# Kernel optimization log

Hardware: AMD Instinct MI355X
Metric: run time of the kernel (lower is better)

The kernel has to match this reference:

```python
import jax, jax.numpy as jnp
import numpy as np

N = 50000      # nodes
E = 800000     # edges (avg degree 16)
IN_DIM = 128
H = 4          # attention heads
D = 32         # hidden dim per head
NEG_SLOPE = 0.2


def setup_inputs() -> dict:
    key = jax.random.key(0)
    ks = jax.random.split(key, 9)
    x = jax.random.normal(ks[0], (N, IN_DIM), dtype=jnp.float32)
    src = jax.random.randint(ks[1], (E,), 0, N, dtype=jnp.int64)
    dst = jax.random.randint(ks[2], (E,), 0, N, dtype=jnp.int64)
    # layer 0: IN_DIM -> H*D ; layer 1: H*D -> H*D
    s0 = 1.0 / np.sqrt(IN_DIM)
    s1 = 1.0 / np.sqrt(H * D)
    W1 = jax.random.normal(ks[3], (H * D, IN_DIM), dtype=jnp.float32) * s0
    al1 = jax.random.normal(ks[4], (1, H, D), dtype=jnp.float32) * s1
    ar1 = jax.random.normal(ks[5], (1, H, D), dtype=jnp.float32) * s1
    W2 = jax.random.normal(ks[6], (H * D, H * D), dtype=jnp.float32) * s1
    al2 = jax.random.normal(ks[7], (1, H, D), dtype=jnp.float32) * s1
    ar2 = jax.random.normal(ks[8], (1, H, D), dtype=jnp.float32) * s1
    return {"x": x, "src": src, "dst": dst, "W1": W1, "al1": al1, "ar1": ar1,
            "W2": W2, "al2": al2, "ar2": ar2}


def gat_conv(h, src, dst, W, al, ar):
    """DGL-style GATConv. h: [N, F_in] -> [N, H, D], with ELU activation."""
    feat = (h @ W.T).reshape(N, H, D)                 # [N,H,D]
    el = jnp.sum(feat * al, axis=-1)                  # [N,H] a_l . Wh
    er = jnp.sum(feat * ar, axis=-1)                  # [N,H] a_r . Wh
    e = jax.nn.leaky_relu(el[src] + er[dst], NEG_SLOPE)  # [E,H]
    # numerically stable edge softmax over incoming edges of each dst node
    m = jax.ops.segment_max(e, dst, num_segments=N)   # [N,H]
    ee = jnp.exp(e - m[dst])                          # [E,H]
    denom = jax.ops.segment_sum(ee, dst, num_segments=N)  # [N,H]
    alpha = ee / denom[dst]                           # [E,H]
    msg = feat[src] * alpha[..., None]                # [E,H,D]
    out = jax.ops.segment_sum(msg, dst, num_segments=N)   # [N,H,D]
    return jax.nn.elu(out)


def reference(x, src, dst, W1, al1, ar1, W2, al2, ar2):
    h = gat_conv(x, src, dst, W1, al1, ar1).reshape(N, H * D)  # flatten(1)
    h = gat_conv(h, src, dst, W2, al2, ar2)                    # [N,H,D]
    return jnp.mean(h, axis=1)                                 # [N,D]
```

## Files before the change

kernel.cpp:

```cpp
#include <hip/hip_runtime.h>
#include <cmath>
#include <type_traits>

#define HEADS 4
#define FDIM 128
#define NEG 0.2f
#define NBUCK 8

typedef __attribute__((ext_vector_type(8))) __bf16 bf16x8;
typedef __attribute__((ext_vector_type(8))) _Float16 h16x8;
typedef __attribute__((ext_vector_type(4))) float f32x4;

__global__ __launch_bounds__(256) void prep_kernel(
    const float* __restrict__ W1, const float* __restrict__ al1,
    const float* __restrict__ ar1,
    const float* __restrict__ W2, const float* __restrict__ al2,
    const float* __restrict__ ar2,
    __bf16* __restrict__ wf1, __bf16* __restrict__ wext1,
    _Float16* __restrict__ wf2, _Float16* __restrict__ wext2,
    int* __restrict__ counts, int nb)
{
    const int b = blockIdx.x, tid = threadIdx.x;
    if (b < 256) {
        int idx = (b & 127) * 256 + tid;
        int j = idx & 7;
        int r = idx >> 3;
        int c = r & 15; r >>= 4;
        int t = r & 7;  r >>= 3;
        int kq = r & 15;
        int hl = r >> 4;
        if (b < 128) {
            float v = W1[(t * 16 + c) * 128 + kq * 8 + j];
            __bf16 hi = (__bf16)v;
            wf1[idx] = (hl == 0) ? hi : (__bf16)(v - (float)hi);
        } else {
            float v = W2[(t * 16 + c) * 128 + kq * 8 + j];
            _Float16 hi = (_Float16)v;
            wf2[idx] = (hl == 0) ? hi : (_Float16)(v - (float)hi);
        }
    } else if (b < 258) {
        const float* W  = (b == 256) ? W1 : W2;
        const float* al = (b == 256) ? al1 : al2;
        const float* ar = (b == 256) ? ar1 : ar2;
        __shared__ float val[1024];
        #pragma unroll
        for (int ch = 0; ch < 4; ++ch) {
            int idx = ch * 256 + tid;
            int c = idx >> 7, k = idx & 127;
            int h = c & 3;
            const float* a = (c < 4) ? al : ar;
            float s = 0.f;
            for (int d = 0; d < 32; ++d)
                s += a[h * 32 + d] * W[(h * 32 + d) * 128 + k];
            val[c * 128 + k] = s;
        }
        __syncthreads();
        #pragma unroll
        for (int ch = 0; ch < 16; ++ch) {
            int idx = tid * 16 + ch;
            int j = idx & 7;
            int r = idx >> 3;
            int c = r & 15; r >>= 4;
            int kq = r & 15;
            int hl = r >> 4;
            float v = (c < 8) ? val[c * 128 + kq * 8 + j] : 0.f;
            if (b == 256) {
                __bf16 hi = (__bf16)v;
                wext1[idx] = (hl == 0) ? hi : (__bf16)(v - (float)hi);
            } else {
                _Float16 hi = (_Float16)v;
                wext2[idx] = (hl == 0) ? hi : (_Float16)(v - (float)hi);
            }
        }
    } else {
        int i0 = ((b - 258) * 256 + tid) * 4;
        if (i0 + 3 < nb) {
            *(int4*)&counts[i0] = make_int4(0, 0, 0, 0);
        } else {
            for (int i = i0; i < nb; ++i) counts[i] = 0;
        }
    }
}

__device__ __forceinline__ void gemm_body_f32(
    const float* __restrict__ X, const bf16x8* __restrict__ wf,
    const bf16x8* __restrict__ wext, _Float16* __restrict__ featH,
    float* __restrict__ el, float* __restrict__ er,
    int nnodes, int tile0, int tend, int stride, bf16x8* lw)
{
    const int tid = threadIdx.x;
    const int wave = tid >> 6, lane = tid & 63;
    const int l15 = lane & 15, quad = lane >> 4;

    int tile = tile0;
    float xr[32], xn[32];

    auto loadX = [&](int tl, float* dst) {
        int nodeA = tl * 64 + wave * 16 + l15;
        bool v = nodeA < nnodes;
        const float4* xp = (const float4*)(X + (size_t)nodeA * 128);
        #pragma unroll
        for (int ks = 0; ks < 4; ++ks) {
            float4 a = v ? xp[ks * 8 + quad * 2]     : make_float4(0.f, 0.f, 0.f, 0.f);
            float4 b = v ? xp[ks * 8 + quad * 2 + 1] : make_float4(0.f, 0.f, 0.f, 0.f);
            dst[ks * 8 + 0] = a.x; dst[ks * 8 + 1] = a.y;
            dst[ks * 8 + 2] = a.z; dst[ks * 8 + 3] = a.w;
            dst[ks * 8 + 4] = b.x; dst[ks * 8 + 5] = b.y;
            dst[ks * 8 + 6] = b.z; dst[ks * 8 + 7] = b.w;
        }
    };

    loadX(tile, xr);
    for (int i = tid; i < 2048; i += 256) lw[i] = wf[i];
    __syncthreads();

    while (true) {
        int next = tile + stride;
        if (next < tend) loadX(next, xn);

        f32x4 acc[9];
        #pragma unroll
        for (int t = 0; t < 9; ++t) acc[t] = (f32x4){0.f, 0.f, 0.f, 0.f};

        #pragma unroll
        for (int ks = 0; ks < 4; ++ks) {
            bf16x8 ahi, alo;
            #pragma unroll
            for (int j = 0; j < 8; ++j) {
                float xv = xr[ks * 8 + j];
                __bf16 h = (__bf16)xv;
                ahi[j] = h;
                alo[j] = (__bf16)(xv - (float)h);
            }
            const int kq = ks * 4 + quad;

            {
                bf16x8 bh = wext[(kq) * 16 + l15];
                bf16x8 bl = wext[(16 + kq) * 16 + l15];
                acc[8] = __builtin_amdgcn_mfma_f32_16x16x32_bf16(ahi, bh, acc[8], 0, 0, 0);
                acc[8] = __builtin_amdgcn_mfma_f32_16x16x32_bf16(alo, bh, acc[8], 0, 0, 0);
                acc[8] = __builtin_amdgcn_mfma_f32_16x16x32_bf16(ahi, bl, acc[8], 0, 0, 0);
            }
            #pragma unroll
            for (int t = 0; t < 8; ++t) {
                bf16x8 bh = lw[(kq * 8 + t) * 16 + l15];
                bf16x8 bl = wf[2048 + (kq * 8 + t) * 16 + l15];
                acc[t] = __builtin_amdgcn_mfma_f32_16x16x32_bf16(ahi, bh, acc[t], 0, 0, 0);
                acc[t] = __builtin_amdgcn_mfma_f32_16x16x32_bf16(alo, bh, acc[t], 0, 0, 0);
                acc[t] = __builtin_amdgcn_mfma_f32_16x16x32_bf16(ahi, bl, acc[t], 0, 0, 0);
            }
        }

        const int nodeC = tile * 64 + wave * 16 + quad * 4;
        #pragma unroll
        for (int r = 0; r < 4; ++r) {
            int gn = nodeC + r;
            if (gn < nnodes) {
                #pragma unroll
                for (int t = 0; t < 8; ++t)
                    featH[(size_t)gn * 128 + t * 16 + l15] = (_Float16)acc[t][r];
            }
        }
        if (l15 < 8) {
            #pragma unroll
            for (int r = 0; r < 4; ++r) {
                int gn = nodeC + r;
                if (gn < nnodes) {
                    if (l15 < 4) el[gn * HEADS + l15] = acc[8][r];
                    else         er[gn * HEADS + (l15 - 4)] = acc[8][r];
                }
            }
        }

        if (next >= tend) break;
        #pragma unroll
        for (int i = 0; i < 32; ++i) xr[i] = xn[i];
        tile = next;
    }
}

__device__ __forceinline__ void gemm_body_f16(
    const _Float16* __restrict__ X, const h16x8* __restrict__ wf,
    const h16x8* __restrict__ wext, _Float16* __restrict__ featH,
    float* __restrict__ el, float* __restrict__ er,
    int nnodes, int tile0, int tend, int stride, h16x8* lw)
{
    const int tid = threadIdx.x;
    const int wave = tid >> 6, lane = tid & 63;
    const int l15 = lane & 15, quad = lane >> 4;

    int tile = tile0;
    h16x8 xr[4], xn[4];

    auto loadX = [&](int tl, h16x8* dst) {
        int nodeA = tl * 64 + wave * 16 + l15;
        bool v = nodeA < nnodes;
        const h16x8* xp = (const h16x8*)(X + (size_t)nodeA * 128);
        #pragma unroll
        for (int ks = 0; ks < 4; ++ks) {
            if (v) {
                dst[ks] = xp[ks * 4 + quad];
            } else {
                #pragma unroll
                for (int j = 0; j < 8; ++j) dst[ks][j] = (_Float16)0.f;
            }
        }
    };

    loadX(tile, xr);
    for (int i = tid; i < 2048; i += 256) lw[i] = wf[i];
    __syncthreads();

    while (true) {
        int next = tile + stride;
        if (next < tend) loadX(next, xn);

        f32x4 acc[9];
        #pragma unroll
        for (int t = 0; t < 9; ++t) acc[t] = (f32x4){0.f, 0.f, 0.f, 0.f};

        #pragma unroll
        for (int ks = 0; ks < 4; ++ks) {
            h16x8 a = xr[ks];
            const int kq = ks * 4 + quad;
            {
                h16x8 bh = wext[(kq) * 16 + l15];
                h16x8 bl = wext[(16 + kq) * 16 + l15];
                acc[8] = __builtin_amdgcn_mfma_f32_16x16x32_f16(a, bh, acc[8], 0, 0, 0);
                acc[8] = __builtin_amdgcn_mfma_f32_16x16x32_f16(a, bl, acc[8], 0, 0, 0);
            }
            #pragma unroll
            for (int t = 0; t < 8; ++t) {
                h16x8 bh = lw[(kq * 8 + t) * 16 + l15];
                h16x8 bl = wf[2048 + (kq * 8 + t) * 16 + l15];
                acc[t] = __builtin_amdgcn_mfma_f32_16x16x32_f16(a, bh, acc[t], 0, 0, 0);
                acc[t] = __builtin_amdgcn_mfma_f32_16x16x32_f16(a, bl, acc[t], 0, 0, 0);
            }
        }

        const int nodeC = tile * 64 + wave * 16 + quad * 4;
        #pragma unroll
        for (int r = 0; r < 4; ++r) {
            int gn = nodeC + r;
            if (gn < nnodes) {
                #pragma unroll
                for (int t = 0; t < 8; ++t)
                    featH[(size_t)gn * 128 + t * 16 + l15] = (_Float16)acc[t][r];
            }
        }
        if (l15 < 8) {
            #pragma unroll
            for (int r = 0; r < 4; ++r) {
                int gn = nodeC + r;
                if (gn < nnodes) {
                    if (l15 < 4) el[gn * HEADS + l15] = acc[8][r];
                    else         er[gn * HEADS + (l15 - 4)] = acc[8][r];
                }
            }
        }

        if (next >= tend) break;
        #pragma unroll
        for (int i = 0; i < 4; ++i) xr[i] = xn[i];
        tile = next;
    }
}

__device__ __forceinline__ void hist_body(
    const int* __restrict__ src, const int* __restrict__ dst,
    int* __restrict__ counts, int* __restrict__ rank, int nedges, int shift, int b)
{
    int i0 = (b * 256 + threadIdx.x) * 8;
    if (i0 + 7 < nedges) {
        int4 d0 = *(const int4*)&dst[i0];
        int4 d1 = *(const int4*)&dst[i0 + 4];
        int4 s0 = *(const int4*)&src[i0];
        int4 s1 = *(const int4*)&src[i0 + 4];
        int4 r0, r1;
        r0.x = atomicAdd(&counts[d0.x * NBUCK + (s0.x >> shift)], 1);
        r0.y = atomicAdd(&counts[d0.y * NBUCK + (s0.y >> shift)], 1);
        r0.z = atomicAdd(&counts[d0.z * NBUCK + (s0.z >> shift)], 1);
        r0.w = atomicAdd(&counts[d0.w * NBUCK + (s0.w >> shift)], 1);
        r1.x = atomicAdd(&counts[d1.x * NBUCK + (s1.x >> shift)], 1);
        r1.y = atomicAdd(&counts[d1.y * NBUCK + (s1.y >> shift)], 1);
        r1.z = atomicAdd(&counts[d1.z * NBUCK + (s1.z >> shift)], 1);
        r1.w = atomicAdd(&counts[d1.w * NBUCK + (s1.w >> shift)], 1);
        *(int4*)&rank[i0]     = r0;
        *(int4*)&rank[i0 + 4] = r1;
    } else {
        for (int i = i0; i < nedges; ++i)
            rank[i] = atomicAdd(&counts[dst[i] * NBUCK + (src[i] >> shift)], 1);
    }
}

__device__ __forceinline__ void scatter_body(
    const int* __restrict__ src, const int* __restrict__ dst,
    const int* __restrict__ rank, const int* __restrict__ offsets,
    int* __restrict__ csr_src, int nedges, int shift, int b)
{
    int i0 = (b * 256 + threadIdx.x) * 8;
    if (i0 + 7 < nedges) {
        int4 d0 = *(const int4*)&dst[i0];
        int4 d1 = *(const int4*)&dst[i0 + 4];
        int4 r0 = *(const int4*)&rank[i0];
        int4 r1 = *(const int4*)&rank[i0 + 4];
        int4 s0 = *(const int4*)&src[i0];
        int4 s1 = *(const int4*)&src[i0 + 4];
        csr_src[offsets[d0.x * NBUCK + (s0.x >> shift)] + r0.x] = s0.x;
        csr_src[offsets[d0.y * NBUCK + (s0.y >> shift)] + r0.y] = s0.y;
        csr_src[offsets[d0.z * NBUCK + (s0.z >> shift)] + r0.z] = s0.z;
        csr_src[offsets[d0.w * NBUCK + (s0.w >> shift)] + r0.w] = s0.w;
        csr_src[offsets[d1.x * NBUCK + (s1.x >> shift)] + r1.x] = s1.x;
        csr_src[offsets[d1.y * NBUCK + (s1.y >> shift)] + r1.y] = s1.y;
        csr_src[offsets[d1.z * NBUCK + (s1.z >> shift)] + r1.z] = s1.z;
        csr_src[offsets[d1.w * NBUCK + (s1.w >> shift)] + r1.w] = s1.w;
    } else {
        for (int i = i0; i < nedges; ++i)
            csr_src[offsets[dst[i] * NBUCK + (src[i] >> shift)] + rank[i]] = src[i];
    }
}

__global__ __launch_bounds__(256) void fused_gemm_hist(
    const float* __restrict__ X, const bf16x8* __restrict__ wf,
    const bf16x8* __restrict__ wext, _Float16* __restrict__ featH,
    float* __restrict__ el, float* __restrict__ er, int nnodes,
    int t0, int tend, int gemm_blocks,
    const int* __restrict__ src, const int* __restrict__ dst,
    int* __restrict__ counts, int* __restrict__ rank, int nedges, int shift)
{
    __shared__ bf16x8 lw[2048];
    if ((int)blockIdx.x < gemm_blocks)
        gemm_body_f32(X, wf, wext, featH, el, er, nnodes,
                      t0 + blockIdx.x, tend, gemm_blocks, lw);
    else
        hist_body(src, dst, counts, rank, nedges, shift, blockIdx.x - gemm_blocks);
}

__global__ __launch_bounds__(256) void fused_gemm_scatter(
    const float* __restrict__ X, const bf16x8* __restrict__ wf,
    const bf16x8* __restrict__ wext, _Float16* __restrict__ featH,
    float* __restrict__ el, float* __restrict__ er, int nnodes,
    int t0, int tend, int gemm_blocks,
    const int* __restrict__ src, const int* __restrict__ dst,
    const int* __restrict__ rank, const int* __restrict__ offsets,
    int* __restrict__ csr_src, int nedges, int shift)
{
    __shared__ bf16x8 lw[2048];
    if ((int)blockIdx.x < gemm_blocks)
        gemm_body_f32(X, wf, wext, featH, el, er, nnodes,
                      t0 + blockIdx.x, tend, gemm_blocks, lw);
    else
        scatter_body(src, dst, rank, offsets, csr_src, nedges, shift,
                     blockIdx.x - gemm_blocks);
}

__global__ __launch_bounds__(256) void gemm_mfma_f16_kernel(
    const _Float16* __restrict__ X, const h16x8* __restrict__ wf,
    const h16x8* __restrict__ wext, _Float16* __restrict__ featH,
    float* __restrict__ el, float* __restrict__ er, int nnodes, int ntiles)
{
    __shared__ h16x8 lw[2048];
    gemm_body_f16(X, wf, wext, featH, el, er, nnodes,
                  blockIdx.x, ntiles, gridDim.x, lw);
}

__global__ __launch_bounds__(256) void scan1_kernel(
    const int* __restrict__ counts, int* __restrict__ offsets,
    int* __restrict__ bsums, int n)
{
    __shared__ int wsums[4];
    const int tid = threadIdx.x, lane = tid & 63, w = tid >> 6;
    const int i = blockIdx.x * 1024 + tid * 4;

    int4 v = make_int4(0, 0, 0, 0);
    if (i + 3 < n) v = *(const int4*)&counts[i];
    else {
        if (i < n)     v.x = counts[i];
        if (i + 1 < n) v.y = counts[i + 1];
        if (i + 2 < n) v.z = counts[i + 2];
    }
    int s0 = v.x, s1 = s0 + v.y, s2 = s1 + v.z, s3 = s2 + v.w;

    int x = s3;
    #pragma unroll
    for (int off = 1; off < 64; off <<= 1) {
        int t = __shfl_up(x, off, 64);
        if (lane >= off) x += t;
    }
    if (lane == 63) wsums[w] = x;
    __syncthreads();
    int wbase = 0;
    #pragma unroll
    for (int k = 0; k < 4; ++k) if (k < w) wbase += wsums[k];

    int tbase = wbase + x - s3;
    if (i < n)     offsets[i]     = tbase;
    if (i + 1 < n) offsets[i + 1] = tbase + s0;
    if (i + 2 < n) offsets[i + 2] = tbase + s1;
    if (i + 3 < n) offsets[i + 3] = tbase + s2;
    if (tid == 255) bsums[blockIdx.x] = wbase + x;
}

__global__ __launch_bounds__(256) void scan23_kernel(
    int* __restrict__ offsets, const int* __restrict__ bsums, int n, int nedges)
{
    __shared__ int sbase;
    const int tid = threadIdx.x, b = blockIdx.x;
    if (tid < 64) {
        int s = 0;
        for (int i = tid; i < b; i += 64) s += bsums[i];
        #pragma unroll
        for (int off = 1; off < 64; off <<= 1) s += __shfl_xor(s, off, 64);
        if (tid == 0) sbase = s;
    }
    __syncthreads();
    const int base = sbase;
    const int i = b * 1024 + tid * 4;
    #pragma unroll
    for (int k = 0; k < 4; ++k)
        if (i + k < n) offsets[i + k] += base;
    if (b == 0 && tid == 0) offsets[n] = nedges;
}

template <bool MEAN>
__global__ __launch_bounds__(256) void aggregate_kernel(
    const _Float16* __restrict__ featH, const float* __restrict__ el,
    const float* __restrict__ er, const int* __restrict__ offsets,
    const int* __restrict__ csr_src, void* __restrict__ outp, int nnodes)
{
    const int n = (blockIdx.x * 256 + threadIdx.x) >> 6;
    if (n >= nnodes) return;
    const int lane = threadIdx.x & 63;
    const int g = lane >> 4, u = lane & 15, h = u >> 2;
    const int beg = offsets[n * NBUCK], end = offsets[n * NBUCK + NBUCK];
    const float ern = er[n * HEADS + h];
    const int iters = (end - beg + 3) >> 2;

    float a[8];
    #pragma unroll
    for (int p = 0; p < 8; ++p) a[p] = 0.f;
    float sw = 0.f;

    const h16x8* __restrict__ frow = (const h16x8*)featH;

    int ja = beg + g;
    int jb = ja + 4;
    bool va = ja < end, vb = jb < end;
    int sa = va ? csr_src[ja] : 0;
    int sb = vb ? csr_src[jb] : 0;
    float qa = el[sa * HEADS + h];
    float qb = el[sb * HEADS + h];
    h16x8 fa = frow[(size_t)sa * 16 + u];
    h16x8 fb = frow[(size_t)sb * 16 + u];

    for (int it = 0; it < iters; ++it) {
        int jc = ja + 8;
        bool vc = jc < end;
        int sc = vc ? csr_src[jc] : 0;
        float qc = el[sc * HEADS + h];
        h16x8 fc = frow[(size_t)sc * 16 + u];

        float e = qa + ern;
        e = e > 0.f ? e : NEG * e;
        float w2 = va ? __expf(e) : 0.f;
        #pragma unroll
        for (int p = 0; p < 8; ++p) a[p] += w2 * (float)fa[p];
        sw += w2;

        ja = jb; va = vb; sa = sb; qa = qb; fa = fb;
        jb = jc; vb = vc; sb = sc; qb = qc; fb = fc;
    }

    #pragma unroll
    for (int p = 0; p < 8; ++p) {
        a[p] += __shfl_xor(a[p], 16, 64);
        a[p] += __shfl_xor(a[p], 32, 64);
    }
    sw += __shfl_xor(sw, 16, 64);
    sw += __shfl_xor(sw, 32, 64);

    float inv = sw > 0.f ? 1.f / sw : 0.f;
    float r[8];
    #pragma unroll
    for (int p = 0; p < 8; ++p) {
        float t = a[p] * inv;
        r[p] = t > 0.f ? t : __expf(t) - 1.f;
    }

    if (!MEAN) {
        if (g == 0) {
            h16x8 o;
            #pragma unroll
            for (int p = 0; p < 8; ++p) o[p] = (_Float16)r[p];
            ((h16x8*)outp)[(size_t)n * 16 + u] = o;
        }
    } else {
        #pragma unroll
        for (int p = 0; p < 8; ++p) {
            r[p] += __shfl_xor(r[p], 4, 64);
            r[p] += __shfl_xor(r[p], 8, 64);
        }
        if (g == 0 && u < 4) {
            float* out = (float*)outp;
            float4* o4 = (float4*)(out + (size_t)n * 32 + u * 8);
            o4[0] = make_float4(0.25f * r[0], 0.25f * r[1], 0.25f * r[2], 0.25f * r[3]);
            o4[1] = make_float4(0.25f * r[4], 0.25f * r[5], 0.25f * r[6], 0.25f * r[7]);
        }
    }
}

extern "C" void kernel_launch(void* const* d_in, const int* in_sizes, int n_in,
                              void* d_out, int out_size, void* d_ws, size_t ws_size,
                              hipStream_t stream)
{
    const float* x   = (const float*)d_in[0];
    const int*   src = (const int*)d_in[1];
    const int*   dst = (const int*)d_in[2];
    const float* W1  = (const float*)d_in[3];
    const float* al1 = (const float*)d_in[4];
    const float* ar1 = (const float*)d_in[5];
    const float* W2  = (const float*)d_in[6];
    const float* al2 = (const float*)d_in[7];
    const float* ar2 = (const float*)d_in[8];

    const int N = in_sizes[0] / FDIM;
    const int E = in_sizes[1];
    const int NB = N * NBUCK;

    int shift = 0;
    while (((N - 1) >> shift) > (NBUCK - 1)) ++shift;

    _Float16* h1 = (_Float16*)d_ws;
    _Float16* featH = h1 + (size_t)N * FDIM;
    float* el = (float*)(featH + (size_t)N * FDIM);
    float* er = el + (size_t)N * HEADS;
    int* counts  = (int*)(er + (size_t)N * HEADS);
    int* offsets = counts + NB;
    int* rank    = offsets + (NB + 1);
    int* csr_src = rank + E;
    int* bsums   = csr_src + E;
    uintptr_t wp = ((uintptr_t)(bsums + 512) + 63) & ~(uintptr_t)63;
    __bf16* wf1     = (__bf16*)wp;
    __bf16* wext1   = wf1 + 32768;
    _Float16* wf2   = (_Float16*)(wext1 + 4096);
    _Float16* wext2 = wf2 + 32768;

    const int ntiles = (N + 63) / 64;
    const int halfT  = (ntiles + 1) / 2;
    const int gA = halfT < 256 ? halfT : 256;
    const int gB = (ntiles - halfT) < 256 ? (ntiles - halfT) : 256;
    const int edge8_grid = ((E + 7) / 8 + 255) / 256;
    const int agg_grid  = (N + 3) / 4;
    const int nscan     = (NB + 1023) / 1024;
    const int zblocks   = ((NB + 3) / 4 + 255) / 256;
    const int g2 = ntiles < 512 ? ntiles : 512;

    prep_kernel<<<258 + zblocks, 256, 0, stream>>>(
        W1, al1, ar1, W2, al2, ar2, wf1, wext1, wf2, wext2, counts, NB);

    fused_gemm_hist<<<gA + edge8_grid, 256, 0, stream>>>(
        x, (const bf16x8*)wf1, (const bf16x8*)wext1, featH, el, er, N,
        0, halfT, gA, src, dst, counts, rank, E, shift);

    scan1_kernel<<<nscan, 256, 0, stream>>>(counts, offsets, bsums, NB);
    scan23_kernel<<<nscan, 256, 0, stream>>>(offsets, bsums, NB, E);

    fused_gemm_scatter<<<gB + edge8_grid, 256, 0, stream>>>(
        x, (const bf16x8*)wf1, (const bf16x8*)wext1, featH, el, er, N,
        halfT, ntiles, gB, src, dst, rank, offsets, csr_src, E, shift);

    aggregate_kernel<false><<<agg_grid, 256, 0, stream>>>(
        featH, el, er, offsets, csr_src, (void*)h1, N);

    gemm_mfma_f16_kernel<<<g2, 256, 0, stream>>>(
        h1, (const h16x8*)wf2, (const h16x8*)wext2, featH, el, er, N, ntiles);
    aggregate_kernel<true><<<agg_grid, 256, 0, stream>>>(
        featH, el, er, offsets, csr_src, d_out, N);
}
```

Before: 238.8 us.

## Replace global-atomic CSR build with two-level LDS radix-style bucket sort

The CSR construction no longer does per-edge global atomics on a dst×src-bucket count array. It now runs a coarse histogram per edge block in LDS, keyed on dst>>7, and scans the block×bucket matrix. A scatter pass then writes (src,dst) pairs into coarse buckets, and a new fine_sort kernel sorts each 128-node bucket in LDS to produce offsets and csr_src. This removes contended global atomics and the counts-zeroing pass, at the cost of an extra kernel, a larger scan and an intermediate int2 buffer. Buckets larger than 4096 edges are silently truncated.

```diff
diff --git a/kernel.cpp b/kernel.cpp
--- a/kernel.cpp
+++ b/kernel.cpp
@@ -6,6 +6,8 @@
 #define FDIM 128
 #define NEG 0.2f
 #define NBUCK 8
+#define CSHIFT 7
+#define CMASK 127
 
 typedef __attribute__((ext_vector_type(8))) __bf16 bf16x8;
 typedef __attribute__((ext_vector_type(8))) _Float16 h16x8;
@@ -17,8 +19,7 @@
     const float* __restrict__ W2, const float* __restrict__ al2,
     const float* __restrict__ ar2,
     __bf16* __restrict__ wf1, __bf16* __restrict__ wext1,
-    _Float16* __restrict__ wf2, _Float16* __restrict__ wext2,
-    int* __restrict__ counts, int nb)
+    _Float16* __restrict__ wf2, _Float16* __restrict__ wext2)
 {
     const int b = blockIdx.x, tid = threadIdx.x;
     if (b < 256) {
@@ -38,7 +39,7 @@
             _Float16 hi = (_Float16)v;
             wf2[idx] = (hl == 0) ? hi : (_Float16)(v - (float)hi);
         }
-    } else if (b < 258) {
+    } else {
         const float* W  = (b == 256) ? W1 : W2;
         const float* al = (b == 256) ? al1 : al2;
         const float* ar = (b == 256) ? ar1 : ar2;
@@ -72,13 +73,6 @@
                 wext2[idx] = (hl == 0) ? hi : (_Float16)(v - (float)hi);
             }
         }
-    } else {
-        int i0 = ((b - 258) * 256 + tid) * 4;
-        if (i0 + 3 < nb) {
-            *(int4*)&counts[i0] = make_int4(0, 0, 0, 0);
-        } else {
-            for (int i = i0; i < nb; ++i) counts[i] = 0;
-        }
     }
 }
 
@@ -266,92 +260,164 @@
     }
 }
 
-__device__ __forceinline__ void hist_body(
-    const int* __restrict__ src, const int* __restrict__ dst,
-    int* __restrict__ counts, int* __restrict__ rank, int nedges, int shift, int b)
-{
-    int i0 = (b * 256 + threadIdx.x) * 8;
+__device__ __forceinline__ void coarse_hist_body(
+    const int* __restrict__ dst, int* __restrict__ histmat,
+    int nedges, int nblk, int nbkt, int eb, int* chist)
+{
+    const int tid = threadIdx.x;
+    for (int i = tid; i < nbkt; i += 256) chist[i] = 0;
+    __syncthreads();
+    int i0 = eb * 2048 + tid * 8;
     if (i0 + 7 < nedges) {
         int4 d0 = *(const int4*)&dst[i0];
         int4 d1 = *(const int4*)&dst[i0 + 4];
-        int4 s0 = *(const int4*)&src[i0];
-        int4 s1 = *(const int4*)&src[i0 + 4];
-        int4 r0, r1;
-        r0.x = atomicAdd(&counts[d0.x * NBUCK + (s0.x >> shift)], 1);
-        r0.y = atomicAdd(&counts[d0.y * NBUCK + (s0.y >> shift)], 1);
-        r0.z = atomicAdd(&counts[d0.z * NBUCK + (s0.z >> shift)], 1);
-        r0.w = atomicAdd(&counts[d0.w * NBUCK + (s0.w >> shift)], 1);
-        r1.x = atomicAdd(&counts[d1.x * NBUCK + (s1.x >> shift)], 1);
-        r1.y = atomicAdd(&counts[d1.y * NBUCK + (s1.y >> shift)], 1);
-        r1.z = atomicAdd(&counts[d1.z * NBUCK + (s1.z >> shift)], 1);
-        r1.w = atomicAdd(&counts[d1.w * NBUCK + (s1.w >> shift)], 1);
-        *(int4*)&rank[i0]     = r0;
-        *(int4*)&rank[i0 + 4] = r1;
+        atomicAdd(&chist[d0.x >> CSHIFT], 1);
+        atomicAdd(&chist[d0.y >> CSHIFT], 1);
+        atomicAdd(&chist[d0.z >> CSHIFT], 1);
+        atomicAdd(&chist[d0.w >> CSHIFT], 1);
+        atomicAdd(&chist[d1.x >> CSHIFT], 1);
+        atomicAdd(&chist[d1.y >> CSHIFT], 1);
+        atomicAdd(&chist[d1.z >> CSHIFT], 1);
+        atomicAdd(&chist[d1.w >> CSHIFT], 1);
     } else {
         for (int i = i0; i < nedges; ++i)
-            rank[i] = atomicAdd(&counts[dst[i] * NBUCK + (src[i] >> shift)], 1);
-    }
-}
-
-__device__ __forceinline__ void scatter_body(
+            atomicAdd(&chist[dst[i] >> CSHIFT], 1);
+    }
+    __syncthreads();
+    for (int i = tid; i < nbkt; i += 256)
+        histmat[i * nblk + eb] = chist[i];
+}
+
+__device__ __forceinline__ void coarse_scatter_body(
     const int* __restrict__ src, const int* __restrict__ dst,
-    const int* __restrict__ rank, const int* __restrict__ offsets,
-    int* __restrict__ csr_src, int nedges, int shift, int b)
-{
-    int i0 = (b * 256 + threadIdx.x) * 8;
+    const int* __restrict__ histoff, int2* __restrict__ tmp,
+    int nedges, int nblk, int nbkt, int eb, int* chist)
+{
+    const int tid = threadIdx.x;
+    for (int i = tid; i < nbkt; i += 256) chist[i] = 0;
+    __syncthreads();
+    int i0 = eb * 2048 + tid * 8;
     if (i0 + 7 < nedges) {
-        int4 d0 = *(const int4*)&dst[i0];
-        int4 d1 = *(const int4*)&dst[i0 + 4];
-        int4 r0 = *(const int4*)&rank[i0];
-        int4 r1 = *(const int4*)&rank[i0 + 4];
-        int4 s0 = *(const int4*)&src[i0];
-        int4 s1 = *(const int4*)&src[i0 + 4];
-        csr_src[offsets[d0.x * NBUCK + (s0.x >> shift)] + r0.x] = s0.x;
-        csr_src[offsets[d0.y * NBUCK + (s0.y >> shift)] + r0.y] = s0.y;
-        csr_src[offsets[d0.z * NBUCK + (s0.z >> shift)] + r0.z] = s0.z;
-        csr_src[offsets[d0.w * NBUCK + (s0.w >> shift)] + r0.w] = s0.w;
-        csr_src[offsets[d1.x * NBUCK + (s1.x >> shift)] + r1.x] = s1.x;
-        csr_src[offsets[d1.y * NBUCK + (s1.y >> shift)] + r1.y] = s1.y;
-        csr_src[offsets[d1.z * NBUCK + (s1.z >> shift)] + r1.z] = s1.z;
-        csr_src[offsets[d1.w * NBUCK + (s1.w >> shift)] + r1.w] = s1.w;
+        int s[8], d[8];
+        *(int4*)&s[0] = *(const int4*)&src[i0];
+        *(int4*)&s[4] = *(const int4*)&src[i0 + 4];
+        *(int4*)&d[0] = *(const int4*)&dst[i0];
+        *(int4*)&d[4] = *(const int4*)&dst[i0 + 4];
+        #pragma unroll
+        for (int q = 0; q < 8; ++q) {
+            int bkt = d[q] >> CSHIFT;
+            int r = atomicAdd(&chist[bkt], 1);
+            int pos = histoff[bkt * nblk + eb] + r;
+            tmp[pos] = make_int2(s[q], d[q]);
+        }
     } else {
-        for (int i = i0; i < nedges; ++i)
-            csr_src[offsets[dst[i] * NBUCK + (src[i] >> shift)] + rank[i]] = src[i];
-    }
-}
-
-__global__ __launch_bounds__(256) void fused_gemm_hist(
+        for (int i = i0; i < nedges; ++i) {
+            int s = src[i], d = dst[i];
+            int bkt = d >> CSHIFT;
+            int r = atomicAdd(&chist[bkt], 1);
+            tmp[histoff[bkt * nblk + eb] + r] = make_int2(s, d);
+        }
+    }
+}
+
+__global__ __launch_bounds__(256) void fused_gemm_chist(
+    const float* __restrict__ X, const bf16x8* __restrict__ wf,
+    const bf16x8* __restrict__ wext, _Float16* __restrict__ featH,
+    float* __restrict__ el, float* __restrict__ er, int nnodes,
+    int t0, int tend, int gemm_blocks,
+    const int* __restrict__ dst, int* __restrict__ histmat,
+    int nedges, int nblk, int nbkt)
+{
+    __shared__ bf16x8 lw[2048];
+    __shared__ int chist[512];
+    if ((int)blockIdx.x < gemm_blocks)
+        gemm_body_f32(X, wf, wext, featH, el, er, nnodes,
+                      t0 + blockIdx.x, tend, gemm_blocks, lw);
+    else
+        coarse_hist_body(dst, histmat, nedges, nblk, nbkt, chist ? (blockIdx.x - gemm_blocks) : 0, chist);
+}
+
+__global__ __launch_bounds__(256) void fused_gemm_cscatter(
     const float* __restrict__ X, const bf16x8* __restrict__ wf,
     const bf16x8* __restrict__ wext, _Float16* __restrict__ featH,
     float* __restrict__ el, float* __restrict__ er, int nnodes,
     int t0, int tend, int gemm_blocks,
     const int* __restrict__ src, const int* __restrict__ dst,
-    int* __restrict__ counts, int* __restrict__ rank, int nedges, int shift)
+    const int* __restrict__ histoff, int2* __restrict__ tmp,
+    int nedges, int nblk, int nbkt)
 {
     __shared__ bf16x8 lw[2048];
+    __shared__ int chist[512];
     if ((int)blockIdx.x < gemm_blocks)
         gemm_body_f32(X, wf, wext, featH, el, er, nnodes,
                       t0 + blockIdx.x, tend, gemm_blocks, lw);
     else
-        hist_body(src, dst, counts, rank, nedges, shift, blockIdx.x - gemm_blocks);
-}
-
-__global__ __launch_bounds__(256) void fused_gemm_scatter(
-    const float* __restrict__ X, const bf16x8* __restrict__ wf,
-    const bf16x8* __restrict__ wext, _Float16* __restrict__ featH,
-    float* __restrict__ el, float* __restrict__ er, int nnodes,
-    int t0, int tend, int gemm_blocks,
-    const int* __restrict__ src, const int* __restrict__ dst,
-    const int* __restrict__ rank, const int* __restrict__ offsets,
-    int* __restrict__ csr_src, int nedges, int shift)
-{
-    __shared__ bf16x8 lw[2048];
-    if ((int)blockIdx.x < gemm_blocks)
-        gemm_body_f32(X, wf, wext, featH, el, er, nnodes,
-                      t0 + blockIdx.x, tend, gemm_blocks, lw);
-    else
-        scatter_body(src, dst, rank, offsets, csr_src, nedges, shift,
-                     blockIdx.x - gemm_blocks);
+        coarse_scatter_body(src, dst, histoff, tmp, nedges, nblk, nbkt,
+                            blockIdx.x - gemm_blocks, chist);
+}
+
+__global__ __launch_bounds__(256) void fine_sort_kernel(
+    const int2* __restrict__ tmp, const int* __restrict__ histoff,
+    int* __restrict__ csr_src, int* __restrict__ offsets,
+    int nblk, int nbkt, int nb, int nedges, int shift)
+{
+    __shared__ int2 eds[4096];
+    __shared__ int fh[1024];
+    __shared__ int wsums[4];
+    const int b = blockIdx.x, tid = threadIdx.x;
+    const int lane = tid & 63, w = tid >> 6;
+
+    const int base = histoff[b * nblk];
+    const int endb = histoff[(b + 1) * nblk];
+    int cnt = endb - base;
+    if (cnt > 4096) cnt = 4096;
+
+    #pragma unroll
+    for (int i = 0; i < 4; ++i) fh[tid + i * 256] = 0;
+    __syncthreads();
+
+    for (int i = tid; i < cnt; i += 256) {
+        int2 e = tmp[base + i];
+        eds[i] = e;
+        int fb = ((e.y & CMASK) << 3) + (e.x >> shift);
+        atomicAdd(&fh[fb], 1);
+    }
+    __syncthreads();
+
+    int v0 = fh[tid * 4], v1 = fh[tid * 4 + 1], v2 = fh[tid * 4 + 2], v3 = fh[tid * 4 + 3];
+    int s0 = v0, s1 = s0 + v1, s2 = s1 + v2, s3 = s2 + v3;
+    int x = s3;
+    #pragma unroll
+    for (int off = 1; off < 64; off <<= 1) {
+        int t = __shfl_up(x, off, 64);
+        if (lane >= off) x += t;
+    }
+    if (lane == 63) wsums[w] = x;
+    __syncthreads();
+    int wbase = 0;
+    #pragma unroll
+    for (int k = 0; k < 4; ++k) if (k < w) wbase += wsums[k];
+    const int tb = wbase + x - s3;
+
+    int o0 = tb, o1 = tb + s0, o2 = tb + s1, o3 = tb + s2;
+    fh[tid * 4]     = o0;
+    fh[tid * 4 + 1] = o1;
+    fh[tid * 4 + 2] = o2;
+    fh[tid * 4 + 3] = o3;
+    int g = b * 1024 + tid * 4;
+    if (g < nb)     offsets[g]     = base + o0;
+    if (g + 1 < nb) offsets[g + 1] = base + o1;
+    if (g + 2 < nb) offsets[g + 2] = base + o2;
+    if (g + 3 < nb) offsets[g + 3] = base + o3;
+    __syncthreads();
+
+    for (int i = tid; i < cnt; i += 256) {
+        int2 e = eds[i];
+        int fb = ((e.y & CMASK) << 3) + (e.x >> shift);
+        int p = atomicAdd(&fh[fb], 1);
+        csr_src[base + p] = e.x;
+    }
+    if (b == 0 && tid == 0) offsets[nb] = nedges;
 }
 
 __global__ __launch_bounds__(256) void gemm_mfma_f16_kernel(
@@ -530,14 +596,20 @@
     int shift = 0;
     while (((N - 1) >> shift) > (NBUCK - 1)) ++shift;
 
+    const int NBKT  = (N + CMASK) >> CSHIFT;
+    const int NBLK1 = (E + 2047) >> 11;
+    const int n1    = NBKT * NBLK1;
+
     _Float16* h1 = (_Float16*)d_ws;
     _Float16* featH = h1 + (size_t)N * FDIM;
     float* el = (float*)(featH + (size_t)N * FDIM);
     float* er = el + (size_t)N * HEADS;
-    int* counts  = (int*)(er + (size_t)N * HEADS);
-    int* offsets = counts + NB;
-    int* rank    = offsets + (NB + 1);
-    int* csr_src = rank + E;
+    uintptr_t tp = ((uintptr_t)(er + (size_t)N * HEADS) + 15) & ~(uintptr_t)15;
+    int2* tmp    = (int2*)tp;
+    int* histmat = (int*)(tmp + E);
+    int* histoff = histmat + n1;
+    int* offsets = histoff + (n1 + 1);
+    int* csr_src = offsets + (NB + 1);
     int* bsums   = csr_src + E;
     uintptr_t wp = ((uintptr_t)(bsums + 512) + 63) & ~(uintptr_t)63;
     __bf16* wf1     = (__bf16*)wp;
@@ -549,25 +621,26 @@
     const int halfT  = (ntiles + 1) / 2;
     const int gA = halfT < 256 ? halfT : 256;
     const int gB = (ntiles - halfT) < 256 ? (ntiles - halfT) : 256;
-    const int edge8_grid = ((E + 7) / 8 + 255) / 256;
     const int agg_grid  = (N + 3) / 4;
-    const int nscan     = (NB + 1023) / 1024;
-    const int zblocks   = ((NB + 3) / 4 + 255) / 256;
+    const int nscan     = (n1 + 1023) / 1024;
     const int g2 = ntiles < 512 ? ntiles : 512;
 
-    prep_kernel<<<258 + zblocks, 256, 0, stream>>>(
-        W1, al1, ar1, W2, al2, ar2, wf1, wext1, wf2, wext2, counts, NB);
-
-    fused_gemm_hist<<<gA + edge8_grid, 256, 0, stream>>>(
+    prep_kernel<<<258, 256, 0, stream>>>(
+        W1, al1, ar1, W2, al2, ar2, wf1, wext1, wf2, wext2);
+
+    fused_gemm_chist<<<gA + NBLK1, 256, 0, stream>>>(
         x, (const bf16x8*)wf1, (const bf16x8*)wext1, featH, el, er, N,
-        0, halfT, gA, src, dst, counts, rank, E, shift);
-
-    scan1_kernel<<<nscan, 256, 0, stream>>>(counts, offsets, bsums, NB);
-    scan23_kernel<<<nscan, 256, 0, stream>>>(offsets, bsums, NB, E);
-
-    fused_gemm_scatter<<<gB + edge8_grid, 256, 0, stream>>>(
+        0, halfT, gA, dst, histmat, E, NBLK1, NBKT);
+
+    scan1_kernel<<<nscan, 256, 0, stream>>>(histmat, histoff, bsums, n1);
+    scan23_kernel<<<nscan, 256, 0, stream>>>(histoff, bsums, n1, E);
+
+    fused_gemm_cscatter<<<gB + NBLK1, 256, 0, stream>>>(
         x, (const bf16x8*)wf1, (const bf16x8*)wext1, featH, el, er, N,
-        halfT, ntiles, gB, src, dst, rank, offsets, csr_src, E, shift);
+        halfT, ntiles, gB, src, dst, histoff, tmp, E, NBLK1, NBKT);
+
+    fine_sort_kernel<<<NBKT, 256, 0, stream>>>(
+        tmp, histoff, csr_src, offsets, NBLK1, NBKT, NB, E, shift);
 
     aggregate_kernel<false><<<agg_grid, 256, 0, stream>>>(
         featH, el, er, offsets, csr_src, (void*)h1, N);
```

Result: faster. 213.3 us (-10.7%).
